# Optimization experiments

Hardware: AMD Instinct MI355X
Metric: run time of the kernel (lower is better)

Reference implementation:

```python
import jax, jax.numpy as jnp
import numpy as np

N_NODES = 50000
N_EDGES = 800000
IN_CH = 256
OUT_CH = 64
HEADS = 4
NEG_SLOPE = 0.2


def setup_inputs() -> dict:
    key = jax.random.key(0)
    k = jax.random.split(key, 7)
    x = jax.random.normal(k[0], (N_NODES, IN_CH), dtype=jnp.float32)
    edge_index = jax.random.randint(k[1], (2, N_EDGES), 0, N_NODES, dtype=jnp.int32)
    # Glorot-style init for the linear projection and attention vectors
    W = jax.random.normal(k[2], (IN_CH, HEADS * OUT_CH), dtype=jnp.float32) / np.sqrt(IN_CH)
    att_src = jax.random.normal(k[3], (HEADS, OUT_CH), dtype=jnp.float32) / np.sqrt(OUT_CH)
    att_dst = jax.random.normal(k[4], (HEADS, OUT_CH), dtype=jnp.float32) / np.sqrt(OUT_CH)
    bias = jnp.zeros((HEADS * OUT_CH,), dtype=jnp.float32)
    return {"x": x, "edge_index": edge_index, "W": W,
            "att_src": att_src, "att_dst": att_dst, "bias": bias}


def reference(x, edge_index, W, att_src, att_dst, bias):
    N = x.shape[0]
    # PyG GATConv default: add self-loops
    loop = jnp.arange(N, dtype=edge_index.dtype)
    src = jnp.concatenate([edge_index[0], loop])
    dst = jnp.concatenate([edge_index[1], loop])

    h = (x @ W).reshape(N, HEADS, OUT_CH)          # [N,H,C]
    a_src = jnp.einsum('nhc,hc->nh', h, att_src)    # [N,H]
    a_dst = jnp.einsum('nhc,hc->nh', h, att_dst)    # [N,H]

    alpha = a_src[src] + a_dst[dst]                 # [E,H]
    alpha = jax.nn.leaky_relu(alpha, NEG_SLOPE)

    # segment softmax over edges grouped by destination node
    amax = jax.ops.segment_max(alpha, dst, num_segments=N)
    amax = jnp.where(jnp.isfinite(amax), amax, 0.0)
    e = jnp.exp(alpha - amax[dst])
    denom = jax.ops.segment_sum(e, dst, num_segments=N)
    coef = e / (denom[dst] + 1e-16)                 # [E,H]

    msg = coef[..., None] * h[src]                  # [E,H,C]
    out = jax.ops.segment_sum(msg, dst, num_segments=N)  # [N,H,C]
    out = out.reshape(N, HEADS * OUT_CH) + bias
    return jax.nn.relu(out)
```

## Files before the change

kernel.cpp:

```cpp
#include <hip/hip_runtime.h>
#include <hip/hip_bf16.h>

#define HC 256
#define NEG_SLOPE 0.2f
#define BM 64
#define BK 64
#define LDK 72

typedef short short8_t __attribute__((ext_vector_type(8)));
typedef float float4_t __attribute__((ext_vector_type(4)));

__device__ __forceinline__ unsigned short f2bf(float f) {
  unsigned u = __float_as_uint(f);
  return (unsigned short)((u + 0x7fffu + ((u >> 16) & 1u)) >> 16);
}
__device__ __forceinline__ float bf2f(unsigned short b) {
  return __uint_as_float(((unsigned)b) << 16);
}

__global__ void wt_kernel(const float* __restrict__ W, unsigned short* __restrict__ Wt)
{
  const int k = blockIdx.x;
  const int n = threadIdx.x;
  Wt[n * 256 + k] = f2bf(W[k * 256 + n]);
}

__global__ __launch_bounds__(256) void gemm_mfma(
    const float* __restrict__ x, const unsigned short* __restrict__ Wt,
    const float* __restrict__ att_src, const float* __restrict__ att_dst,
    unsigned short* __restrict__ h, float* __restrict__ a_src,
    float* __restrict__ a_dst, int nnodes)
{
  __shared__ unsigned short As[BM * LDK];
  __shared__ unsigned short Bs[256 * LDK];
  const int t    = threadIdx.x;
  const int wv   = t >> 6;
  const int lane = t & 63;
  const int r0   = blockIdx.x * BM;

  float4_t acc[4][4] = {};

  for (int k0 = 0; k0 < 256; k0 += BK) {
    __syncthreads();
    {
      const int row = t >> 2, kc = (t & 3) * 16;
      const int gr = r0 + row;
      float4 xv[4];
      if (gr < nnodes) {
        const float4* p = (const float4*)(x + (size_t)gr * 256 + k0 + kc);
        xv[0] = p[0]; xv[1] = p[1]; xv[2] = p[2]; xv[3] = p[3];
      } else {
        xv[0] = xv[1] = xv[2] = xv[3] = make_float4(0.f, 0.f, 0.f, 0.f);
      }
      const float* f = (const float*)xv;
      unsigned pk[8];
      #pragma unroll
      for (int i = 0; i < 8; ++i) {
        __hip_bfloat162 b2 = __float22bfloat162_rn(make_float2(f[2 * i], f[2 * i + 1]));
        pk[i] = *(unsigned*)&b2;
      }
      uint4* d = (uint4*)&As[row * LDK + kc];
      d[0] = make_uint4(pk[0], pk[1], pk[2], pk[3]);
      d[1] = make_uint4(pk[4], pk[5], pk[6], pk[7]);
    }
    #pragma unroll
    for (int it = 0; it < 4; ++it) {
      const int n = it * 64 + (t >> 2);
      const int kc = (t & 3) * 16;
      const uint4* g = (const uint4*)(Wt + (size_t)n * 256 + k0 + kc);
      uint4 v0 = g[0], v1 = g[1];
      uint4* d = (uint4*)&Bs[n * LDK + kc];
      d[0] = v0; d[1] = v1;
    }
    __syncthreads();

    #pragma unroll
    for (int ks = 0; ks < 2; ++ks) {
      const int ko = ks * 32 + (lane >> 4) * 8;
      short8_t af[4], bfr[4];
      #pragma unroll
      for (int mt = 0; mt < 4; ++mt)
        af[mt] = *(const short8_t*)&As[(16 * mt + (lane & 15)) * LDK + ko];
      #pragma unroll
      for (int nt = 0; nt < 4; ++nt)
        bfr[nt] = *(const short8_t*)&Bs[(64 * wv + 16 * nt + (lane & 15)) * LDK + ko];
      #pragma unroll
      for (int mt = 0; mt < 4; ++mt)
        #pragma unroll
        for (int nt = 0; nt < 4; ++nt)
          acc[mt][nt] = __builtin_amdgcn_mfma_f32_16x16x32_bf16(
              af[mt], bfr[nt], acc[mt][nt], 0, 0, 0);
    }
  }

  const int q = lane >> 4, l15 = lane & 15;
  float atts[4], attd[4];
  #pragma unroll
  for (int nt = 0; nt < 4; ++nt) {
    atts[nt] = att_src[wv * 64 + 16 * nt + l15];
    attd[nt] = att_dst[wv * 64 + 16 * nt + l15];
  }

  #pragma unroll
  for (int mt = 0; mt < 4; ++mt) {
    #pragma unroll
    for (int reg = 0; reg < 4; ++reg) {
      const int row = r0 + 16 * mt + 4 * q + reg;
      const bool ok = row < nnodes;
      float ps = 0.f, pd = 0.f;
      #pragma unroll
      for (int nt = 0; nt < 4; ++nt) {
        const float v = acc[mt][nt][reg];
        if (ok) h[(size_t)row * 256 + 64 * wv + 16 * nt + l15] = f2bf(v);
        ps += v * atts[nt];
        pd += v * attd[nt];
      }
      #pragma unroll
      for (int off = 8; off; off >>= 1) {
        ps += __shfl_down(ps, off, 16);
        pd += __shfl_down(pd, off, 16);
      }
      if (ok && l15 == 0) {
        a_src[row * 4 + wv] = ps;
        a_dst[row * 4 + wv] = pd;
      }
    }
  }
}

__global__ void deg_count(const int* __restrict__ ei, int* __restrict__ deg, int E)
{
  const int e = blockIdx.x * blockDim.x + threadIdx.x;
  if (e >= E) return;
  atomicAdd(&deg[ei[E + e]], 1);
}

__global__ __launch_bounds__(256) void scan_p1(const int* __restrict__ deg,
                                               int* __restrict__ bsum, int n)
{
  __shared__ int ws[4];
  const int t = threadIdx.x, lane = t & 63, wv = t >> 6;
  const int base = blockIdx.x * 1024 + t * 4;
  int4 v = make_int4(0, 0, 0, 0);
  if (base + 3 < n) v = *(const int4*)&deg[base];
  else {
    if (base + 0 < n) v.x = deg[base + 0];
    if (base + 1 < n) v.y = deg[base + 1];
    if (base + 2 < n) v.z = deg[base + 2];
  }
  int s = (v.x + v.y) + (v.z + v.w);
  #pragma unroll
  for (int off = 32; off; off >>= 1) s += __shfl_down(s, off, 64);
  if (lane == 0) ws[wv] = s;
  __syncthreads();
  if (t == 0) bsum[blockIdx.x] = (ws[0] + ws[1]) + (ws[2] + ws[3]);
}

__global__ __launch_bounds__(1024) void scan_p2(const int* __restrict__ bsum,
                                                int* __restrict__ boff,
                                                int* __restrict__ rowptr,
                                                int nb, int n)
{
  __shared__ int wsum[16], woff[16];
  const int t = threadIdx.x, lane = t & 63, wv = t >> 6;
  int v = (t < nb) ? bsum[t] : 0;
  int sc = v;
  #pragma unroll
  for (int off = 1; off < 64; off <<= 1) {
    int u = __shfl_up(sc, off, 64);
    if (lane >= off) sc += u;
  }
  if (lane == 63) wsum[wv] = sc;
  __syncthreads();
  if (t == 0) {
    int run = 0;
    #pragma unroll
    for (int i = 0; i < 16; ++i) { int x = wsum[i]; woff[i] = run; run += x; }
    rowptr[n] = run;
  }
  __syncthreads();
  if (t < nb) boff[t] = woff[wv] + sc - v;
}

__global__ __launch_bounds__(256) void scan_p3(const int* __restrict__ deg,
                                               const int* __restrict__ boff,
                                               int* __restrict__ rowptr,
                                               int* __restrict__ cursor, int n)
{
  __shared__ int wsum[4], woff[4];
  const int t = threadIdx.x, lane = t & 63, wv = t >> 6;
  const int base = blockIdx.x * 1024 + t * 4;
  int4 v = make_int4(0, 0, 0, 0);
  if (base + 3 < n) v = *(const int4*)&deg[base];
  else {
    if (base + 0 < n) v.x = deg[base + 0];
    if (base + 1 < n) v.y = deg[base + 1];
    if (base + 2 < n) v.z = deg[base + 2];
  }
  const int s = (v.x + v.y) + (v.z + v.w);
  int sc = s;
  #pragma unroll
  for (int off = 1; off < 64; off <<= 1) {
    int u = __shfl_up(sc, off, 64);
    if (lane >= off) sc += u;
  }
  if (lane == 63) wsum[wv] = sc;
  __syncthreads();
  if (t == 0) {
    int run = 0;
    #pragma unroll
    for (int i = 0; i < 4; ++i) { int x = wsum[i]; woff[i] = run; run += x; }
  }
  __syncthreads();
  int excl = boff[blockIdx.x] + woff[wv] + (sc - s);
  int4 r;
  r.x = excl;
  r.y = r.x + v.x;
  r.z = r.y + v.y;
  r.w = r.z + v.z;
  if (base + 3 < n) {
    *(int4*)&rowptr[base] = r;
    *(int4*)&cursor[base] = r;
  } else {
    if (base + 0 < n) { rowptr[base + 0] = r.x; cursor[base + 0] = r.x; }
    if (base + 1 < n) { rowptr[base + 1] = r.y; cursor[base + 1] = r.y; }
    if (base + 2 < n) { rowptr[base + 2] = r.z; cursor[base + 2] = r.z; }
  }
}

__global__ __launch_bounds__(256) void fill_csr(
    const int* __restrict__ ei, const float* __restrict__ a_src,
    const float* __restrict__ a_dst, int* __restrict__ cursor,
    int* __restrict__ csr_src, float4* __restrict__ wexp, int E, int nnodes)
{
  const int g    = blockIdx.x & 7;
  const int bg   = blockIdx.x >> 3;
  const int nbg  = gridDim.x >> 3;
  const int gsz  = (nnodes + 7) >> 3;
  const int dlo  = g * gsz;
  const int dhi  = min(dlo + gsz, nnodes);

  for (int e = bg * 256 + threadIdx.x; e < E; e += nbg * 256) {
    const int d = ei[E + e];
    if (d < dlo || d >= dhi) continue;
    const int s = ei[e];
    const int pos = atomicAdd(&cursor[d], 1);
    csr_src[pos] = s;
    const float4 as = ((const float4*)a_src)[s];
    const float4 ad = ((const float4*)a_dst)[d];
    float4 al;
    al.x = as.x + ad.x; al.y = as.y + ad.y;
    al.z = as.z + ad.z; al.w = as.w + ad.w;
    al.x = al.x > 0.f ? al.x : NEG_SLOPE * al.x;
    al.y = al.y > 0.f ? al.y : NEG_SLOPE * al.y;
    al.z = al.z > 0.f ? al.z : NEG_SLOPE * al.z;
    al.w = al.w > 0.f ? al.w : NEG_SLOPE * al.w;
    al.x = expf(al.x); al.y = expf(al.y); al.z = expf(al.z); al.w = expf(al.w);
    wexp[pos] = al;
  }
}

__device__ __forceinline__ float4 ld_h(const unsigned short* __restrict__ h,
                                       int row, int cb)
{
  const ushort4 u = *(const ushort4*)&h[(size_t)row * 256 + cb];
  return make_float4(bf2f(u.x), bf2f(u.y), bf2f(u.z), bf2f(u.w));
}

__global__ __launch_bounds__(256) void gather_kernel(
    const int* __restrict__ rowptr, const int* __restrict__ csr_src,
    const float* __restrict__ wexp, const unsigned short* __restrict__ h,
    const float* __restrict__ a_src, const float* __restrict__ a_dst,
    const float* __restrict__ bias, float* __restrict__ out, int n)
{
  const int wave = threadIdx.x >> 6;
  const int lane = threadIdx.x & 63;
  const int d = blockIdx.x * 4 + wave;
  if (d >= n) return;

  const int head = lane >> 4;
  const int cb   = lane * 4;

  float alpha = a_src[d * 4 + head] + a_dst[d * 4 + head];
  alpha = alpha > 0.f ? alpha : NEG_SLOPE * alpha;
  float w = expf(alpha);
  float dsum = w;
  float4 hv = ld_h(h, d, cb);
  float4 acc = make_float4(w * hv.x, w * hv.y, w * hv.z, w * hv.w);

  int j = rowptr[d];
  const int end = rowptr[d + 1];

  for (; j + 3 < end; j += 4) {
    const int4 s4 = *(const int4*)&csr_src[j];
    const float w0 = wexp[(j + 0) * 4 + head];
    const float w1 = wexp[(j + 1) * 4 + head];
    const float w2 = wexp[(j + 2) * 4 + head];
    const float w3 = wexp[(j + 3) * 4 + head];
    const float4 h0 = ld_h(h, s4.x, cb);
    const float4 h1 = ld_h(h, s4.y, cb);
    const float4 h2 = ld_h(h, s4.z, cb);
    const float4 h3 = ld_h(h, s4.w, cb);
    dsum += (w0 + w1) + (w2 + w3);
    acc.x += w0 * h0.x + w1 * h1.x + w2 * h2.x + w3 * h3.x;
    acc.y += w0 * h0.y + w1 * h1.y + w2 * h2.y + w3 * h3.y;
    acc.z += w0 * h0.z + w1 * h1.z + w2 * h2.z + w3 * h3.z;
    acc.w += w0 * h0.w + w1 * h1.w + w2 * h2.w + w3 * h3.w;
  }
  for (; j < end; ++j) {
    const int s0 = csr_src[j];
    const float w0 = wexp[j * 4 + head];
    const float4 h0 = ld_h(h, s0, cb);
    dsum += w0;
    acc.x += w0 * h0.x; acc.y += w0 * h0.y;
    acc.z += w0 * h0.z; acc.w += w0 * h0.w;
  }

  const float inv = 1.f / (dsum + 1e-16f);
  const float4 b4 = ((const float4*)bias)[lane];
  float4 o;
  o.x = acc.x * inv + b4.x; o.x = o.x > 0.f ? o.x : 0.f;
  o.y = acc.y * inv + b4.y; o.y = o.y > 0.f ? o.y : 0.f;
  o.z = acc.z * inv + b4.z; o.z = o.z > 0.f ? o.z : 0.f;
  o.w = acc.w * inv + b4.w; o.w = o.w > 0.f ? o.w : 0.f;
  *(float4*)&out[(size_t)d * 256 + cb] = o;
}

extern "C" void kernel_launch(void* const* d_in, const int* in_sizes, int n_in,
                              void* d_out, int out_size, void* d_ws, size_t ws_size,
                              hipStream_t stream)
{
  const float* x       = (const float*)d_in[0];
  const int*   ei      = (const int*)d_in[1];
  const float* W       = (const float*)d_in[2];
  const float* att_src = (const float*)d_in[3];
  const float* att_dst = (const float*)d_in[4];
  const float* bias    = (const float*)d_in[5];

  const int nnodes = in_sizes[0] / HC;
  const int E      = in_sizes[1] / 2;
  const int nb     = (nnodes + 1023) / 1024;

  float* out = (float*)d_out;
  char* ws = (char*)d_ws;
  unsigned short* h  = (unsigned short*)ws;
  float* a_src = (float*)(ws + (size_t)nnodes * HC * 2);
  float* a_dst = a_src + (size_t)nnodes * 4;
  unsigned short* Wt = (unsigned short*)(a_dst + (size_t)nnodes * 4);
  int* deg    = (int*)((char*)Wt + 256 * 256 * 2);
  int* rowptr = deg + nnodes;
  int* cursor = rowptr + ((nnodes + 1 + 3) & ~3);
  int* bsum   = cursor + nnodes;
  int* boff   = bsum + ((nb + 3) & ~3);
  float4* wexp = (float4*)(boff + ((nb + 3) & ~3));
  int* csr    = (int*)(wexp + E);

  hipMemsetAsync(deg, 0, (size_t)nnodes * sizeof(int), stream);

  wt_kernel<<<256, 256, 0, stream>>>(W, Wt);

  gemm_mfma<<<(nnodes + BM - 1) / BM, 256, 0, stream>>>(
      x, Wt, att_src, att_dst, h, a_src, a_dst, nnodes);

  deg_count<<<(E + 255) / 256, 256, 0, stream>>>(ei, deg, E);
  scan_p1<<<nb, 256, 0, stream>>>(deg, bsum, nnodes);
  scan_p2<<<1, 1024, 0, stream>>>(bsum, boff, rowptr, nb, nnodes);
  scan_p3<<<nb, 256, 0, stream>>>(deg, boff, rowptr, cursor, nnodes);

  fill_csr<<<1024, 256, 0, stream>>>(ei, a_src, a_dst, cursor, csr,
                                     (float4*)wexp, E, nnodes);

  gather_kernel<<<(nnodes + 3) / 4, 256, 0, stream>>>(
      rowptr, csr, (const float*)wexp, h, a_src, a_dst, bias, out, nnodes);
}
```

Baseline: 276.9 us.

## Split gather by channel slice with persistent blocks and head-major edge weights

The gather kernel is restructured so each block handles one of 8 column slices of 32 channels, a fixed head, across a grid-stride loop over destination nodes. Within a wave, 4 sub-groups of 16 lanes split a node's edges and combine results by shuffle reduction. Edge weights move to a head-major [4][E] layout so each lane reads one scalar, and csr/weight loads and output stores use nontemporal hints. The intent is to make all blocks sharing a slice reuse the same 64-byte column stripe of h in L2 and to parallelise across edges. The cost is that csr_src and rowptr are re-read 8 times, each h row fetch is narrower, and the cross-lane reduction adds work.

Measured after the change: 525.3 us. 1.9x slower.

```diff
diff --git a/kernel.cpp b/kernel.cpp
--- a/kernel.cpp
+++ b/kernel.cpp
@@ -9,6 +9,7 @@
 
 typedef short short8_t __attribute__((ext_vector_type(8)));
 typedef float float4_t __attribute__((ext_vector_type(4)));
+typedef float float2_t __attribute__((ext_vector_type(2)));
 
 __device__ __forceinline__ unsigned short f2bf(float f) {
   unsigned u = __float_as_uint(f);
@@ -231,7 +232,7 @@
 __global__ __launch_bounds__(256) void fill_csr(
     const int* __restrict__ ei, const float* __restrict__ a_src,
     const float* __restrict__ a_dst, int* __restrict__ cursor,
-    int* __restrict__ csr_src, float4* __restrict__ wexp, int E, int nnodes)
+    int* __restrict__ csr_src, float* __restrict__ wexp, int E, int nnodes)
 {
   const int g    = blockIdx.x & 7;
   const int bg   = blockIdx.x >> 3;
@@ -255,75 +256,66 @@
     al.y = al.y > 0.f ? al.y : NEG_SLOPE * al.y;
     al.z = al.z > 0.f ? al.z : NEG_SLOPE * al.z;
     al.w = al.w > 0.f ? al.w : NEG_SLOPE * al.w;
-    al.x = expf(al.x); al.y = expf(al.y); al.z = expf(al.z); al.w = expf(al.w);
-    wexp[pos] = al;
-  }
-}
-
-__device__ __forceinline__ float4 ld_h(const unsigned short* __restrict__ h,
-                                       int row, int cb)
-{
-  const ushort4 u = *(const ushort4*)&h[(size_t)row * 256 + cb];
-  return make_float4(bf2f(u.x), bf2f(u.y), bf2f(u.z), bf2f(u.w));
+    wexp[pos]         = expf(al.x);
+    wexp[E + pos]     = expf(al.y);
+    wexp[2 * E + pos] = expf(al.z);
+    wexp[3 * E + pos] = expf(al.w);
+  }
 }
 
 __global__ __launch_bounds__(256) void gather_kernel(
     const int* __restrict__ rowptr, const int* __restrict__ csr_src,
-    const float* __restrict__ wexp, const unsigned short* __restrict__ h,
+    const float* __restrict__ wexp_t, const unsigned short* __restrict__ h,
     const float* __restrict__ a_src, const float* __restrict__ a_dst,
-    const float* __restrict__ bias, float* __restrict__ out, int n)
-{
+    const float* __restrict__ bias, float* __restrict__ out, int n, int E)
+{
+  const int g    = blockIdx.x & 7;
+  const int bg   = blockIdx.x >> 3;
+  const int nbg  = gridDim.x >> 3;
   const int wave = threadIdx.x >> 6;
   const int lane = threadIdx.x & 63;
-  const int d = blockIdx.x * 4 + wave;
-  if (d >= n) return;
-
-  const int head = lane >> 4;
-  const int cb   = lane * 4;
-
-  float alpha = a_src[d * 4 + head] + a_dst[d * 4 + head];
-  alpha = alpha > 0.f ? alpha : NEG_SLOPE * alpha;
-  float w = expf(alpha);
-  float dsum = w;
-  float4 hv = ld_h(h, d, cb);
-  float4 acc = make_float4(w * hv.x, w * hv.y, w * hv.z, w * hv.w);
-
-  int j = rowptr[d];
-  const int end = rowptr[d + 1];
-
-  for (; j + 3 < end; j += 4) {
-    const int4 s4 = *(const int4*)&csr_src[j];
-    const float w0 = wexp[(j + 0) * 4 + head];
-    const float w1 = wexp[(j + 1) * 4 + head];
-    const float w2 = wexp[(j + 2) * 4 + head];
-    const float w3 = wexp[(j + 3) * 4 + head];
-    const float4 h0 = ld_h(h, s4.x, cb);
-    const float4 h1 = ld_h(h, s4.y, cb);
-    const float4 h2 = ld_h(h, s4.z, cb);
-    const float4 h3 = ld_h(h, s4.w, cb);
-    dsum += (w0 + w1) + (w2 + w3);
-    acc.x += w0 * h0.x + w1 * h1.x + w2 * h2.x + w3 * h3.x;
-    acc.y += w0 * h0.y + w1 * h1.y + w2 * h2.y + w3 * h3.y;
-    acc.z += w0 * h0.z + w1 * h1.z + w2 * h2.z + w3 * h3.z;
-    acc.w += w0 * h0.w + w1 * h1.w + w2 * h2.w + w3 * h3.w;
-  }
-  for (; j < end; ++j) {
-    const int s0 = csr_src[j];
-    const float w0 = wexp[j * 4 + head];
-    const float4 h0 = ld_h(h, s0, cb);
-    dsum += w0;
-    acc.x += w0 * h0.x; acc.y += w0 * h0.y;
-    acc.z += w0 * h0.z; acc.w += w0 * h0.w;
-  }
-
-  const float inv = 1.f / (dsum + 1e-16f);
-  const float4 b4 = ((const float4*)bias)[lane];
-  float4 o;
-  o.x = acc.x * inv + b4.x; o.x = o.x > 0.f ? o.x : 0.f;
-  o.y = acc.y * inv + b4.y; o.y = o.y > 0.f ? o.y : 0.f;
-  o.z = acc.z * inv + b4.z; o.z = o.z > 0.f ? o.z : 0.f;
-  o.w = acc.w * inv + b4.w; o.w = o.w > 0.f ? o.w : 0.f;
-  *(float4*)&out[(size_t)d * 256 + cb] = o;
+  const int head = g >> 1;
+  const int sub  = lane >> 4;
+  const int cb   = g * 32 + (lane & 15) * 2;
+
+  const float* __restrict__ wrow = wexp_t + (size_t)head * E;
+  const float2_t b2 = *(const float2_t*)&bias[cb];
+
+  for (int d = bg * 4 + wave; d < n; d += nbg * 4) {
+    float alpha = a_src[d * 4 + head] + a_dst[d * 4 + head];
+    alpha = alpha > 0.f ? alpha : NEG_SLOPE * alpha;
+    const float wself = expf(alpha);
+
+    float dsum = 0.f, ax = 0.f, ay = 0.f;
+    if (sub == 0) {
+      const ushort2 u = *(const ushort2*)&h[(size_t)d * 256 + cb];
+      dsum = wself;
+      ax = wself * bf2f(u.x);
+      ay = wself * bf2f(u.y);
+    }
+
+    const int end = rowptr[d + 1];
+    for (int j = rowptr[d] + sub; j < end; j += 4) {
+      const int   s = __builtin_nontemporal_load(&csr_src[j]);
+      const float w = __builtin_nontemporal_load(&wrow[j]);
+      const ushort2 u = *(const ushort2*)&h[(size_t)s * 256 + cb];
+      dsum += w;
+      ax += w * bf2f(u.x);
+      ay += w * bf2f(u.y);
+    }
+
+    dsum += __shfl_xor(dsum, 16); dsum += __shfl_xor(dsum, 32);
+    ax   += __shfl_xor(ax, 16);   ax   += __shfl_xor(ax, 32);
+    ay   += __shfl_xor(ay, 16);   ay   += __shfl_xor(ay, 32);
+
+    if (lane < 16) {
+      const float inv = 1.f / (dsum + 1e-16f);
+      float2_t o;
+      o.x = ax * inv + b2.x; o.x = o.x > 0.f ? o.x : 0.f;
+      o.y = ay * inv + b2.y; o.y = o.y > 0.f ? o.y : 0.f;
+      __builtin_nontemporal_store(o, (float2_t*)&out[(size_t)d * 256 + cb]);
+    }
+  }
 }
 
 extern "C" void kernel_launch(void* const* d_in, const int* in_sizes, int n_in,
@@ -352,8 +344,8 @@
   int* cursor = rowptr + ((nnodes + 1 + 3) & ~3);
   int* bsum   = cursor + nnodes;
   int* boff   = bsum + ((nb + 3) & ~3);
-  float4* wexp = (float4*)(boff + ((nb + 3) & ~3));
-  int* csr    = (int*)(wexp + E);
+  float* wexp = (float*)(boff + ((nb + 3) & ~3));
+  int* csr    = (int*)(wexp + (size_t)4 * E);
 
   hipMemsetAsync(deg, 0, (size_t)nnodes * sizeof(int), stream);
 
@@ -368,8 +360,8 @@
   scan_p3<<<nb, 256, 0, stream>>>(deg, boff, rowptr, cursor, nnodes);
 
   fill_csr<<<1024, 256, 0, stream>>>(ei, a_src, a_dst, cursor, csr,
-                                     (float4*)wexp, E, nnodes);
-
-  gather_kernel<<<(nnodes + 3) / 4, 256, 0, stream>>>(
-      rowptr, csr, (const float*)wexp, h, a_src, a_dst, bias, out, nnodes);
-}
+                                     wexp, E, nnodes);
+
+  gather_kernel<<<8 * 2048, 256, 0, stream>>>(
+      rowptr, csr, wexp, h, a_src, a_dst, bias, out, nnodes, E);
+}
```

## Compute edge attention weights inside gather instead of materializing in CSR fill

Applied to the files above, without the earlier changes.

fill_csr now writes only source indices. It no longer computes leaky-relu/exp edge weights or stores a float4 per edge to a wexp buffer. The gather kernel recomputes each weight on the fly from a_src[src] and a_dst[d], and software-prefetches the next int4 of CSR indices with nontemporal loads. This removes the per-edge float4 write and read-back. In exchange it adds a random a_src gather and an exp per edge per lane in the gather loop.

Result: no change. 275.0 us (-0.7%).

```diff
diff --git a/kernel.cpp b/kernel.cpp
--- a/kernel.cpp
+++ b/kernel.cpp
@@ -9,6 +9,7 @@
 
 typedef short short8_t __attribute__((ext_vector_type(8)));
 typedef float float4_t __attribute__((ext_vector_type(4)));
+typedef int   int4_t   __attribute__((ext_vector_type(4)));
 
 __device__ __forceinline__ unsigned short f2bf(float f) {
   unsigned u = __float_as_uint(f);
@@ -229,9 +230,8 @@
 }
 
 __global__ __launch_bounds__(256) void fill_csr(
-    const int* __restrict__ ei, const float* __restrict__ a_src,
-    const float* __restrict__ a_dst, int* __restrict__ cursor,
-    int* __restrict__ csr_src, float4* __restrict__ wexp, int E, int nnodes)
+    const int* __restrict__ ei, int* __restrict__ cursor,
+    int* __restrict__ csr_src, int E, int nnodes)
 {
   const int g    = blockIdx.x & 7;
   const int bg   = blockIdx.x >> 3;
@@ -243,20 +243,8 @@
   for (int e = bg * 256 + threadIdx.x; e < E; e += nbg * 256) {
     const int d = ei[E + e];
     if (d < dlo || d >= dhi) continue;
-    const int s = ei[e];
     const int pos = atomicAdd(&cursor[d], 1);
-    csr_src[pos] = s;
-    const float4 as = ((const float4*)a_src)[s];
-    const float4 ad = ((const float4*)a_dst)[d];
-    float4 al;
-    al.x = as.x + ad.x; al.y = as.y + ad.y;
-    al.z = as.z + ad.z; al.w = as.w + ad.w;
-    al.x = al.x > 0.f ? al.x : NEG_SLOPE * al.x;
-    al.y = al.y > 0.f ? al.y : NEG_SLOPE * al.y;
-    al.z = al.z > 0.f ? al.z : NEG_SLOPE * al.z;
-    al.w = al.w > 0.f ? al.w : NEG_SLOPE * al.w;
-    al.x = expf(al.x); al.y = expf(al.y); al.z = expf(al.z); al.w = expf(al.w);
-    wexp[pos] = al;
+    csr_src[pos] = ei[e];
   }
 }
 
@@ -267,9 +255,16 @@
   return make_float4(bf2f(u.x), bf2f(u.y), bf2f(u.z), bf2f(u.w));
 }
 
+__device__ __forceinline__ float edge_w(float as, float ad)
+{
+  float al = as + ad;
+  al = al > 0.f ? al : NEG_SLOPE * al;
+  return expf(al);
+}
+
 __global__ __launch_bounds__(256) void gather_kernel(
     const int* __restrict__ rowptr, const int* __restrict__ csr_src,
-    const float* __restrict__ wexp, const unsigned short* __restrict__ h,
+    const unsigned short* __restrict__ h,
     const float* __restrict__ a_src, const float* __restrict__ a_dst,
     const float* __restrict__ bias, float* __restrict__ out, int n)
 {
@@ -281,9 +276,9 @@
   const int head = lane >> 4;
   const int cb   = lane * 4;
 
-  float alpha = a_src[d * 4 + head] + a_dst[d * 4 + head];
-  alpha = alpha > 0.f ? alpha : NEG_SLOPE * alpha;
-  float w = expf(alpha);
+  const float ad = a_dst[d * 4 + head];
+
+  const float w = edge_w(a_src[d * 4 + head], ad);
   float dsum = w;
   float4 hv = ld_h(h, d, cb);
   float4 acc = make_float4(w * hv.x, w * hv.y, w * hv.z, w * hv.w);
@@ -291,25 +286,39 @@
   int j = rowptr[d];
   const int end = rowptr[d + 1];
 
-  for (; j + 3 < end; j += 4) {
-    const int4 s4 = *(const int4*)&csr_src[j];
-    const float w0 = wexp[(j + 0) * 4 + head];
-    const float w1 = wexp[(j + 1) * 4 + head];
-    const float w2 = wexp[(j + 2) * 4 + head];
-    const float w3 = wexp[(j + 3) * 4 + head];
-    const float4 h0 = ld_h(h, s4.x, cb);
-    const float4 h1 = ld_h(h, s4.y, cb);
-    const float4 h2 = ld_h(h, s4.z, cb);
-    const float4 h3 = ld_h(h, s4.w, cb);
+  int4_t sC = {0, 0, 0, 0};
+  if (j + 3 < end)
+    sC = __builtin_nontemporal_load((const int4_t*)&csr_src[j]);
+  while (j + 3 < end) {
+    const int jn = j + 4;
+    const int jp = (jn + 3 < end) ? jn : j;
+    const int4_t sN = __builtin_nontemporal_load((const int4_t*)&csr_src[jp]);
+
+    const float as0 = a_src[sC.x * 4 + head];
+    const float as1 = a_src[sC.y * 4 + head];
+    const float as2 = a_src[sC.z * 4 + head];
+    const float as3 = a_src[sC.w * 4 + head];
+    const float4 h0 = ld_h(h, sC.x, cb);
+    const float4 h1 = ld_h(h, sC.y, cb);
+    const float4 h2 = ld_h(h, sC.z, cb);
+    const float4 h3 = ld_h(h, sC.w, cb);
+
+    const float w0 = edge_w(as0, ad);
+    const float w1 = edge_w(as1, ad);
+    const float w2 = edge_w(as2, ad);
+    const float w3 = edge_w(as3, ad);
+
     dsum += (w0 + w1) + (w2 + w3);
     acc.x += w0 * h0.x + w1 * h1.x + w2 * h2.x + w3 * h3.x;
     acc.y += w0 * h0.y + w1 * h1.y + w2 * h2.y + w3 * h3.y;
     acc.z += w0 * h0.z + w1 * h1.z + w2 * h2.z + w3 * h3.z;
     acc.w += w0 * h0.w + w1 * h1.w + w2 * h2.w + w3 * h3.w;
+
+    sC = sN; j = jn;
   }
   for (; j < end; ++j) {
     const int s0 = csr_src[j];
-    const float w0 = wexp[j * 4 + head];
+    const float w0 = edge_w(a_src[s0 * 4 + head], ad);
     const float4 h0 = ld_h(h, s0, cb);
     dsum += w0;
     acc.x += w0 * h0.x; acc.y += w0 * h0.y;
@@ -352,8 +361,7 @@
   int* cursor = rowptr + ((nnodes + 1 + 3) & ~3);
   int* bsum   = cursor + nnodes;
   int* boff   = bsum + ((nb + 3) & ~3);
-  float4* wexp = (float4*)(boff + ((nb + 3) & ~3));
-  int* csr    = (int*)(wexp + E);
+  int* csr    = boff + ((nb + 3) & ~3);
 
   hipMemsetAsync(deg, 0, (size_t)nnodes * sizeof(int), stream);
 
@@ -367,9 +375,8 @@
   scan_p2<<<1, 1024, 0, stream>>>(bsum, boff, rowptr, nb, nnodes);
   scan_p3<<<nb, 256, 0, stream>>>(deg, boff, rowptr, cursor, nnodes);
 
-  fill_csr<<<1024, 256, 0, stream>>>(ei, a_src, a_dst, cursor, csr,
-                                     (float4*)wexp, E, nnodes);
+  fill_csr<<<1024, 256, 0, stream>>>(ei, cursor, csr, E, nnodes);
 
   gather_kernel<<<(nnodes + 3) / 4, 256, 0, stream>>>(
-      rowptr, csr, (const float*)wexp, h, a_src, a_dst, bias, out, nnodes);
-}
+      rowptr, csr, h, a_src, a_dst, bias, out, nnodes);
+}
```
